# Optimization experiments

Hardware: AMD Instinct MI355X
Metric: run time of the kernel (lower is better)

## Reference

```python
import jax, jax.numpy as jnp
import numpy as np

N = 50000      # nodes
E = 600000     # edges
CIN = 256      # in_channels
H = 4          # heads
C = 64         # hidden_channels (per head)
RATIO = 0.5
K1 = int(np.ceil(RATIO * N))   # 25000
K2 = int(np.ceil(RATIO * K1))  # 12500
NEG = jnp.float32(-1e30)


def gat_conv(x, src, dst, mask, W, a_src, a_dst, b, n):
    """PyG GATConv (concat=True, add_self_loops=True, negative_slope=0.2).
    x: [n, Fin]; src/dst: [e]; mask: [e] bool (invalid edges excluded)."""
    h = (x @ W).reshape(n, H, C)                    # [n, H, C]
    loop = jnp.arange(n, dtype=src.dtype)
    src = jnp.concatenate([src, loop])
    dst = jnp.concatenate([dst, loop])
    mask = jnp.concatenate([mask, jnp.ones((n,), bool)])
    al_s = jnp.sum(h * a_src, axis=-1)              # [n, H]
    al_d = jnp.sum(h * a_dst, axis=-1)              # [n, H]
    e = jax.nn.leaky_relu(al_s[src] + al_d[dst], negative_slope=0.2)  # [e', H]
    e = jnp.where(mask[:, None], e, NEG)
    m = jax.ops.segment_max(e, dst, num_segments=n)                   # [n, H]
    ex = jnp.where(mask[:, None], jnp.exp(e - m[dst]), 0.0)
    den = jax.ops.segment_sum(ex, dst, num_segments=n)                # [n, H]
    alpha = ex / den[dst]                                             # softmax over in-edges
    msg = alpha[:, :, None] * h[src]                                  # [e', H, C]
    out = jax.ops.segment_sum(msg, dst, num_segments=n)               # [n, H, C]
    return out.reshape(n, H * C) + b


def topk_pool(x, src, dst, mask, p, k):
    """PyG TopKPooling: score = tanh(x.p/|p|), keep top-k nodes, gate x by score,
    reindex surviving edges (dropped edges masked out)."""
    score = jnp.tanh((x @ p) / jnp.linalg.norm(p))   # [n]
    sc, perm = jax.lax.top_k(score, k)               # descending, like torch.topk
    x_new = x[perm] * sc[:, None]
    n = x.shape[0]
    inv = jnp.full((n,), -1, jnp.int32).at[perm].set(jnp.arange(k, dtype=jnp.int32))
    ns, nd = inv[src], inv[dst]
    nmask = mask & (ns >= 0) & (nd >= 0)
    ns = jnp.where(nmask, ns, 0)
    nd = jnp.where(nmask, nd, 0)
    return x_new, ns, nd, nmask, perm


def setup_inputs():
    key = jax.random.key(0)
    ks = jax.random.split(key, 14)
    s = 0.05
    return {
        "x": jax.random.normal(ks[0], (N, CIN), jnp.float32),
        "edge_index": jax.random.randint(ks[1], (2, E), 0, N, dtype=jnp.int32),
        "batch": jnp.zeros((N,), jnp.int32),
        "W1": jax.random.normal(ks[2], (CIN, H * C), jnp.float32) * s,
        "a_src1": jax.random.normal(ks[3], (H, C), jnp.float32) * s,
        "a_dst1": jax.random.normal(ks[4], (H, C), jnp.float32) * s,
        "b1": jnp.zeros((H * C,), jnp.float32),
        "p1": jax.random.normal(ks[5], (H * C,), jnp.float32) * s,
        "W2": jax.random.normal(ks[6], (H * C, H * C), jnp.float32) * s,
        "a_src2": jax.random.normal(ks[7], (H, C), jnp.float32) * s,
        "a_dst2": jax.random.normal(ks[8], (H, C), jnp.float32) * s,
        "b2": jnp.zeros((H * C,), jnp.float32),
        "p2": jax.random.normal(ks[9], (H * C,), jnp.float32) * s,
    }


def reference(x, edge_index, batch, W1, a_src1, a_dst1, b1, p1,
              W2, a_src2, a_dst2, b2, p2):
    src, dst = edge_index[0], edge_index[1]
    mask = jnp.ones((E,), bool)
    x1 = gat_conv(x, src, dst, mask, W1, a_src1, a_dst1, b1, N)
    x1, src, dst, mask, perm1 = topk_pool(x1, src, dst, mask, p1, K1)
    x1 = jax.nn.relu(x1)
    batch1 = batch[perm1]
    x2 = gat_conv(x1, src, dst, mask, W2, a_src2, a_dst2, b2, K1)
    x2, src, dst, mask, perm2 = topk_pool(x2, src, dst, mask, p2, K2)
    x2 = jax.nn.relu(x2)
    batch2 = batch1[perm2]
    return (x2, jnp.stack([src, dst]), mask, batch2)
```

## Files before the change

kernel.cpp:

```cpp
#include <hip/hip_runtime.h>
#include <math.h>

typedef unsigned long long ull;

#define NN1 50000
#define EE  600000
#define KK1 25000
#define KK2 12500

#define NB (1<<18)
#define BSHIFT 46

#define CDIV(a,b) (((a)+(b)-1)/(b))

__device__ __forceinline__ ull encd(double d){
  ull u = (ull)__double_as_longlong(d);
  return (u & 0x8000000000000000ULL) ? ~u : (u | 0x8000000000000000ULL);
}
__device__ __forceinline__ double lrelu(double z){ return z > 0.0 ? z : 0.2*z; }

__global__ void zeroi_k(int* __restrict__ p, int n){
  int t = blockIdx.x*blockDim.x + threadIdx.x;
  if (t < n) p[t] = 0;
}
__global__ void zero2_k(int* __restrict__ a, int* __restrict__ b, int n){
  int t = blockIdx.x*blockDim.x + threadIdx.x;
  if (t < n){ a[t] = 0; b[t] = 0; }
}

__global__ void prepq_k(const float* __restrict__ W, const float* __restrict__ as,
                        const float* __restrict__ ad, const float* __restrict__ p,
                        double* __restrict__ Q){
  int k = blockIdx.x; int ch = threadIdx.x; int head = ch>>6; int lane = ch&63;
  double w = (double)W[k*256 + ch];
  double vs = w*(double)as[ch], vd = w*(double)ad[ch], vp = w*(double)p[ch];
  for (int off=32; off; off>>=1){
    vs += __shfl_down(vs,off); vd += __shfl_down(vd,off); vp += __shfl_down(vp,off);
  }
  if (lane==0){ Q[k*12+head]=vs; Q[k*12+4+head]=vd; Q[k*12+8+head]=vp; }
}

template<typename TA>
__global__ __launch_bounds__(256) void matvec_k(const TA* __restrict__ A, const double* __restrict__ Q,
                                                double* __restrict__ als, double* __restrict__ ald,
                                                double* __restrict__ hp, int n){
  __shared__ double P[4][64][13];
  int tid = threadIdx.x;
  int w = tid >> 6, l = tid & 63;
  int base = blockIdx.x*64;
  int r = base + l;
  double acc[12];
  #pragma unroll
  for (int j=0;j<12;j++) acc[j] = 0.0;
  if (r < n){
    const TA*    rowp = A + (size_t)r*256 + w*64;
    const double* qp  = Q + (size_t)w*64*12;
    if constexpr (sizeof(TA)==4){
      #pragma unroll 4
      for (int i=0;i<16;i++){
        float4 v = *reinterpret_cast<const float4*>(rowp + i*4);
        double e0=(double)v.x, e1=(double)v.y, e2=(double)v.z, e3=(double)v.w;
        #pragma unroll
        for (int j=0;j<12;j++) acc[j] = fma(e0, qp[(i*4+0)*12+j], acc[j]);
        #pragma unroll
        for (int j=0;j<12;j++) acc[j] = fma(e1, qp[(i*4+1)*12+j], acc[j]);
        #pragma unroll
        for (int j=0;j<12;j++) acc[j] = fma(e2, qp[(i*4+2)*12+j], acc[j]);
        #pragma unroll
        for (int j=0;j<12;j++) acc[j] = fma(e3, qp[(i*4+3)*12+j], acc[j]);
      }
    } else {
      #pragma unroll 4
      for (int i=0;i<32;i++){
        double2 v = *reinterpret_cast<const double2*>(rowp + i*2);
        #pragma unroll
        for (int j=0;j<12;j++) acc[j] = fma(v.x, qp[(i*2+0)*12+j], acc[j]);
        #pragma unroll
        for (int j=0;j<12;j++) acc[j] = fma(v.y, qp[(i*2+1)*12+j], acc[j]);
      }
    }
  }
  #pragma unroll
  for (int j=0;j<12;j++) P[w][l][j] = acc[j];
  __syncthreads();
  if (tid < 64){
    int rr = base + tid;
    if (rr < n){
      double s[12];
      #pragma unroll
      for (int j=0;j<12;j++)
        s[j] = ((P[0][tid][j] + P[1][tid][j]) + P[2][tid][j]) + P[3][tid][j];
      #pragma unroll
      for (int h=0;h<4;h++){
        als[rr*4+h] = s[h];
        ald[rr*4+h] = s[4+h];
        hp [rr*4+h] = s[8+h];
      }
    }
  }
}

__global__ void deg_k(const int* __restrict__ dst, const int* __restrict__ msk,
                      int* __restrict__ deg, int e){
  int t = blockIdx.x*blockDim.x + threadIdx.x;
  if (t >= e) return;
  if (msk && !msk[t]) return;
  atomicAdd(&deg[dst[t]], 1);
}

__global__ __launch_bounds__(256) void scanA_k(int* __restrict__ a, int* __restrict__ btot, int n){
  __shared__ int s[256];
  int g = blockIdx.x*256 + threadIdx.x;
  s[threadIdx.x] = (g < n) ? a[g] : 0;
  __syncthreads();
  for (int off=1; off<256; off<<=1){
    int t = (threadIdx.x >= off) ? s[threadIdx.x-off] : 0;
    __syncthreads();
    s[threadIdx.x] += t;
    __syncthreads();
  }
  if (g < n) a[g] = s[threadIdx.x];
  if (threadIdx.x == 255) btot[blockIdx.x] = s[255];
}

__global__ __launch_bounds__(1024) void scanB_k(int* __restrict__ btot, int nb){
  __shared__ int s[1024];
  int t = threadIdx.x;
  s[t] = (t < nb) ? btot[t] : 0;
  __syncthreads();
  for (int off=1; off<1024; off<<=1){
    int v = (t >= off) ? s[t-off] : 0;
    __syncthreads();
    s[t] += v;
    __syncthreads();
  }
  if (t < nb) btot[t] = s[t];
}

__global__ void scanC_rowptr_k(const int* __restrict__ a, const int* __restrict__ btot,
                               int* __restrict__ rowptr, int* __restrict__ cursor, int n){
  int g = blockIdx.x*blockDim.x + threadIdx.x;
  if (g >= n) return;
  int B = g >> 8;
  int off = (B > 0) ? btot[B-1] : 0;
  rowptr[g+1] = a[g] + off;
  cursor[g] = 0;
  if (g == 0) rowptr[0] = 0;
}

__global__ void scanC_above_k(const int* __restrict__ a, const int* __restrict__ btot,
                              int* __restrict__ habove, int nelems, int nbins){
  int g = blockIdx.x*blockDim.x + threadIdx.x;
  if (g >= nbins) return;
  int B = g >> 8;
  int off = (B > 0) ? btot[B-1] : 0;
  habove[g] = nelems - (a[g] + off);
}

__global__ void place_k(const int* __restrict__ dst, const int* __restrict__ msk,
                        const int* __restrict__ src, const int* __restrict__ rowptr,
                        int* __restrict__ cursor, int* __restrict__ csr, int e){
  int t = blockIdx.x*blockDim.x + threadIdx.x;
  if (t >= e) return;
  if (msk && !msk[t]) return;
  int d = dst[t];
  int slot = atomicAdd(&cursor[d], 1);
  csr[rowptr[d] + slot] = src[t];
}

__global__ void nodew_k(const double* __restrict__ als, const double* __restrict__ ald,
                        const double* __restrict__ hp, const int* __restrict__ csr,
                        const int* __restrict__ rowptr, const double* __restrict__ nrmbp,
                        double* __restrict__ wse, double* __restrict__ wed,
                        double* __restrict__ z, int n){
  int g = blockIdx.x*blockDim.x + threadIdx.x;
  int i = g>>2, h = g&3;
  if (i >= n) return;
  double aldv = ald[g];
  double selfev = lrelu(als[g] + aldv);
  int b = rowptr[i], e = rowptr[i+1];
  double m = selfev;
  for (int t=b; t<e; t++){
    int s = csr[t];
    double ev = lrelu(als[s*4+h] + aldv);
    m = fmax(m, ev);
  }
  double ws = exp(selfev - m);
  wse[g] = ws;
  double acc = ws * hp[g];
  double den = ws;
  for (int t=b; t<e; t++){
    int s = csr[t];
    double ev = lrelu(als[s*4+h] + aldv);
    double w = exp(ev - m);
    wed[(long)t*4+h] = w;
    acc = fma(w, hp[(long)s*4+h], acc);
    den += w;
  }
  double part = acc/den;
  part += __shfl_xor(part, 1);
  part += __shfl_xor(part, 2);
  if (h == 0) z[i] = (part + nrmbp[1]) / nrmbp[0];
}

template<typename TA>
__global__ void aggx4_k(const TA* __restrict__ X, const int* __restrict__ prm,
                        const int* __restrict__ rowptr, const int* __restrict__ csr,
                        const double* __restrict__ wed, const double* __restrict__ wse,
                        double* __restrict__ Xagg){
  int r = blockIdx.x, k = threadIdx.x;
  int i = prm[r];
  double w0 = wse[i*4+0], w1 = wse[i*4+1], w2 = wse[i*4+2], w3 = wse[i*4+3];
  double xv = (double)X[(long)i*256 + k];
  double a0=w0*xv, a1=w1*xv, a2=w2*xv, a3=w3*xv;
  double d0=w0, d1=w1, d2=w2, d3=w3;
  int b = rowptr[i], e = rowptr[i+1];
  for (int t=b; t<e; t++){
    int s = csr[t];
    double sv = (double)X[(long)s*256 + k];
    double e0=wed[(long)t*4+0], e1=wed[(long)t*4+1];
    double e2=wed[(long)t*4+2], e3=wed[(long)t*4+3];
    a0=fma(e0,sv,a0); a1=fma(e1,sv,a1); a2=fma(e2,sv,a2); a3=fma(e3,sv,a3);
    d0+=e0; d1+=e1; d2+=e2; d3+=e3;
  }
  long base = (long)r*1024 + k;
  Xagg[base      ] = a0/d0;
  Xagg[base + 256] = a1/d1;
  Xagg[base + 512] = a2/d2;
  Xagg[base + 768] = a3/d3;
}

template<typename TO>
__global__ __launch_bounds__(256) void gemmE_k(const double* __restrict__ A,
                                               const float* __restrict__ W,
                                               const float* __restrict__ bias,
                                               const double* __restrict__ scs,
                                               TO* __restrict__ Out, int n){
  __shared__ double As[64][34];
  __shared__ double Bs[32][68];
  int tid = threadIdx.x;
  int r0 = blockIdx.x*64; int head = blockIdx.y; int c0 = head*64;
  int ty = tid>>4, tx = tid&15;
  double acc[4][4] = {};
  for (int k0=0; k0<256; k0+=32){
    int kA = tid&31, rA = tid>>5;
    #pragma unroll
    for (int i=0;i<8;i++){
      int rr = rA + i*8; int gr = r0+rr;
      As[rr][kA] = (gr<n) ? A[(long)gr*1024 + head*256 + k0 + kA] : 0.0;
    }
    int cB = tid&63, kB = tid>>6;
    #pragma unroll
    for (int i=0;i<8;i++){
      int kk = kB + i*4;
      Bs[kk][cB] = (double)W[(k0+kk)*256 + c0 + cB];
    }
    __syncthreads();
    #pragma unroll 4
    for (int k=0;k<32;k+=2){
      double2 a2[4];
      double blo[4], bhi[4];
      #pragma unroll
      for (int i=0;i<4;i++) a2[i] = *reinterpret_cast<const double2*>(&As[ty*4+i][k]);
      #pragma unroll
      for (int j=0;j<4;j++){ blo[j] = Bs[k][tx+16*j]; bhi[j] = Bs[k+1][tx+16*j]; }
      #pragma unroll
      for (int i=0;i<4;i++)
        #pragma unroll
        for (int j=0;j<4;j++) acc[i][j] = fma(a2[i].x, blo[j], acc[i][j]);
      #pragma unroll
      for (int i=0;i<4;i++)
        #pragma unroll
        for (int j=0;j<4;j++) acc[i][j] = fma(a2[i].y, bhi[j], acc[i][j]);
    }
    __syncthreads();
  }
  #pragma unroll
  for (int i=0;i<4;i++){
    int gr = r0 + ty*4 + i;
    if (gr < n){
      double s = scs[gr];
      #pragma unroll
      for (int j=0;j<4;j++){
        int c = c0 + tx + 16*j;
        double v = (acc[i][j] + (double)bias[c]) * s;
        Out[(long)gr*256 + c] = (TO)(v > 0.0 ? v : 0.0);
      }
    }
  }
}

__global__ void pnorm_k(const float* __restrict__ p, const float* __restrict__ bias,
                        double* __restrict__ nrmbp){
  __shared__ double ws_[8];
  int tid = threadIdx.x;
  double pv = (double)p[tid];
  double v = pv*pv;
  double w = (double)bias[tid]*pv;
  for (int off=32; off; off>>=1){ v += __shfl_down(v, off); w += __shfl_down(w, off); }
  if ((tid&63)==0){ ws_[tid>>6] = v; ws_[4+(tid>>6)] = w; }
  __syncthreads();
  if (tid == 0){
    nrmbp[0] = sqrt(ws_[0]+ws_[1]+ws_[2]+ws_[3]);
    nrmbp[1] = ws_[4]+ws_[5]+ws_[6]+ws_[7];
  }
}

__global__ void keyhist_k(const double* __restrict__ z, ull* __restrict__ k64,
                          int* __restrict__ hist, int n){
  int i = blockIdx.x*blockDim.x + threadIdx.x;
  if (i >= n) return;
  ull e = encd(z[i]);
  k64[i] = e;
  atomicAdd(&hist[(int)(e >> BSHIFT)], 1);
}

__global__ void bplace_k(const ull* __restrict__ k64, const int* __restrict__ habove,
                         int* __restrict__ cur, int* __restrict__ isort, int n){
  int i = blockIdx.x*blockDim.x + threadIdx.x;
  if (i >= n) return;
  int b = (int)(k64[i] >> BSHIFT);
  int slot = atomicAdd(&cur[b], 1);
  isort[habove[b] + slot] = i;
}

__global__ void brank_k(const ull* __restrict__ k64, const int* __restrict__ habove,
                        const int* __restrict__ isort, int* __restrict__ rank, int n){
  int i = blockIdx.x*blockDim.x + threadIdx.x;
  if (i >= n) return;
  ull ki = k64[i];
  int b = (int)(ki >> BSHIFT);
  int lo = habove[b];
  int hi = (b > 0) ? habove[b-1] : n;
  int cnt = 0;
  for (int t = lo; t < hi; t++){
    int j = isort[t];
    ull kj = k64[j];
    cnt += ((kj > ki) || (kj == ki && j < i)) ? 1 : 0;
  }
  rank[i] = lo + cnt;
}

__global__ void scatter_k(const double* __restrict__ z, const int* __restrict__ rank,
                          int* __restrict__ perm, int* __restrict__ inv,
                          double* __restrict__ scs, int n, int k){
  int i = blockIdx.x*blockDim.x + threadIdx.x;
  if (i >= n) return;
  int r = rank[i];
  inv[i] = (r < k) ? r : -1;
  if (r < k){ perm[r] = i; scs[r] = tanh(z[i]); }
}

__global__ void reindex_k(const int* __restrict__ src, const int* __restrict__ dst,
                          const int* __restrict__ inv,
                          int* __restrict__ ns, int* __restrict__ nd, int* __restrict__ nmsk, int e){
  int t = blockIdx.x*blockDim.x + threadIdx.x;
  if (t >= e) return;
  int a = inv[src[t]], b = inv[dst[t]];
  int ok = (a >= 0) && (b >= 0);
  ns[t] = ok ? a : 0; nd[t] = ok ? b : 0; nmsk[t] = ok;
}

__global__ void finedge_k(const int* __restrict__ ns, const int* __restrict__ nd,
                          const int* __restrict__ msk, const int* __restrict__ inv,
                          float* __restrict__ osrc, float* __restrict__ odst,
                          float* __restrict__ omsk, int e){
  int t = blockIdx.x*blockDim.x + threadIdx.x;
  if (t >= e) return;
  int a = inv[ns[t]], b = inv[nd[t]];
  int ok = msk[t] && (a >= 0) && (b >= 0);
  osrc[t] = (float)(ok ? a : 0);
  odst[t] = (float)(ok ? b : 0);
  omsk[t] = ok ? 1.0f : 0.0f;
}

__global__ void zerof_k(float* __restrict__ o, int n){
  int t = blockIdx.x*blockDim.x + threadIdx.x;
  if (t < n) o[t] = 0.0f;
}

extern "C" void kernel_launch(void* const* d_in, const int* in_sizes, int n_in,
                              void* d_out, int out_size, void* d_ws, size_t ws_size,
                              hipStream_t stream){
  (void)in_sizes; (void)n_in; (void)out_size; (void)ws_size;
  const float* x   = (const float*)d_in[0];
  const int*   ei  = (const int*)d_in[1];
  const float* W1  = (const float*)d_in[3];
  const float* as1 = (const float*)d_in[4];
  const float* ad1 = (const float*)d_in[5];
  const float* b1  = (const float*)d_in[6];
  const float* p1  = (const float*)d_in[7];
  const float* W2  = (const float*)d_in[8];
  const float* as2 = (const float*)d_in[9];
  const float* ad2 = (const float*)d_in[10];
  const float* b2  = (const float*)d_in[11];
  const float* p2  = (const float*)d_in[12];
  const int* src0 = ei;
  const int* dst0 = ei + EE;

  char* cur_ = (char*)d_ws;
  auto take = [&](size_t bytes)->void*{ void* p = (void*)cur_; cur_ += (bytes + 255) & ~(size_t)255; return p; };
  double* Xagg = (double*)take((size_t)12500*1024*8);
  double* Xi   = (double*)take((size_t)KK1*256*8);
  double* als  = (double*)take((size_t)NN1*4*8);
  double* ald  = (double*)take((size_t)NN1*4*8);
  ull*    menc = (ull*)   take((size_t)NN1*4*8);
  double* wse  = (double*)take((size_t)NN1*4*8);
  double* hp   = (double*)take((size_t)NN1*4*8);
  double* wed  = (double*)take((size_t)EE*4*8);
  double* sco  = (double*)take((size_t)NN1*8);
  double* scs  = (double*)take((size_t)KK1*8);
  double* nrm  = (double*)take(256);
  double* Q    = (double*)take((size_t)3072*8);
  ull*    k64  = (ull*)   take((size_t)NN1*8);
  int* isort= (int*)take((size_t)NN1*4);
  int* rnk  = (int*)take((size_t)NN1*4);
  int* prm  = (int*)take((size_t)KK1*4);
  int* inv  = (int*)take((size_t)NN1*4);
  int* deg  = (int*)take((size_t)(NN1+1)*4);
  int* rwp  = (int*)take((size_t)(NN1+1)*4);
  int* cursr= (int*)take((size_t)NN1*4);
  int* csr  = (int*)take((size_t)EE*4);
  int* ns   = (int*)take((size_t)EE*4);
  int* nd   = (int*)take((size_t)EE*4);
  int* mk2  = (int*)take((size_t)EE*4);
  int* btot = (int*)take((size_t)1024*4);

  int* hist   = (int*)als;
  int* habove = (int*)ald;
  int* bcur   = (int*)menc;

  float* out = (float*)d_out;
  float* o_x = out;
  float* o_s = out + (size_t)KK2*256;
  float* o_d = o_s + EE;
  float* o_m = o_d + EE;
  float* o_b = o_m + EE;

  prepq_k<<<256,256,0,stream>>>(W1, as1, ad1, p1, Q);
  pnorm_k<<<1,256,0,stream>>>(p1, b1, nrm);
  matvec_k<float><<<CDIV(NN1,64),256,0,stream>>>(x, Q, als, ald, hp, NN1);
  zeroi_k<<<CDIV(NN1,256),256,0,stream>>>(deg, NN1);
  deg_k<<<CDIV(EE,256),256,0,stream>>>(dst0, nullptr, deg, EE);
  scanA_k<<<CDIV(NN1,256),256,0,stream>>>(deg, btot, NN1);
  scanB_k<<<1,1024,0,stream>>>(btot, CDIV(NN1,256));
  scanC_rowptr_k<<<CDIV(NN1,256),256,0,stream>>>(deg, btot, rwp, cursr, NN1);
  place_k<<<CDIV(EE,256),256,0,stream>>>(dst0, nullptr, src0, rwp, cursr, csr, EE);
  nodew_k<<<CDIV(NN1*4,256),256,0,stream>>>(als, ald, hp, csr, rwp, nrm, wse, wed, sco, NN1);

  zero2_k<<<NB/256,256,0,stream>>>(hist, bcur, NB);
  keyhist_k<<<CDIV(NN1,256),256,0,stream>>>(sco, k64, hist, NN1);
  scanA_k<<<NB/256,256,0,stream>>>(hist, btot, NB);
  scanB_k<<<1,1024,0,stream>>>(btot, NB/256);
  scanC_above_k<<<NB/256,256,0,stream>>>(hist, btot, habove, NN1, NB);
  bplace_k<<<CDIV(NN1,256),256,0,stream>>>(k64, habove, bcur, isort, NN1);
  brank_k<<<CDIV(NN1,256),256,0,stream>>>(k64, habove, isort, rnk, NN1);
  scatter_k<<<CDIV(NN1,256),256,0,stream>>>(sco, rnk, prm, inv, scs, NN1, KK1);

  aggx4_k<float><<<12500,256,0,stream>>>(x, prm, rwp, csr, wed, wse, Xagg);
  gemmE_k<double><<<dim3(CDIV(12500,64),4),256,0,stream>>>(Xagg, W1, b1, scs, Xi, 12500);
  aggx4_k<float><<<12500,256,0,stream>>>(x, prm+12500, rwp, csr, wed, wse, Xagg);
  gemmE_k<double><<<dim3(CDIV(12500,64),4),256,0,stream>>>(Xagg, W1, b1, scs+12500,
                                                           Xi+(size_t)12500*256, 12500);
  reindex_k<<<CDIV(EE,256),256,0,stream>>>(src0, dst0, inv, ns, nd, mk2, EE);

  prepq_k<<<256,256,0,stream>>>(W2, as2, ad2, p2, Q);
  pnorm_k<<<1,256,0,stream>>>(p2, b2, nrm);
  matvec_k<double><<<CDIV(KK1,64),256,0,stream>>>(Xi, Q, als, ald, hp, KK1);
  zeroi_k<<<CDIV(KK1,256),256,0,stream>>>(deg, KK1);
  deg_k<<<CDIV(EE,256),256,0,stream>>>(nd, mk2, deg, EE);
  scanA_k<<<CDIV(KK1,256),256,0,stream>>>(deg, btot, KK1);
  scanB_k<<<1,1024,0,stream>>>(btot, CDIV(KK1,256));
  scanC_rowptr_k<<<CDIV(KK1,256),256,0,stream>>>(deg, btot, rwp, cursr, KK1);
  place_k<<<CDIV(EE,256),256,0,stream>>>(nd, mk2, ns, rwp, cursr, csr, EE);
  nodew_k<<<CDIV(KK1*4,256),256,0,stream>>>(als, ald, hp, csr, rwp, nrm, wse, wed, sco, KK1);

  zero2_k<<<NB/256,256,0,stream>>>(hist, bcur, NB);
  keyhist_k<<<CDIV(KK1,256),256,0,stream>>>(sco, k64, hist, KK1);
  scanA_k<<<NB/256,256,0,stream>>>(hist, btot, NB);
  scanB_k<<<1,1024,0,stream>>>(btot, NB/256);
  scanC_above_k<<<NB/256,256,0,stream>>>(hist, btot, habove, KK1, NB);
  bplace_k<<<CDIV(KK1,256),256,0,stream>>>(k64, habove, bcur, isort, KK1);
  brank_k<<<CDIV(KK1,256),256,0,stream>>>(k64, habove, isort, rnk, KK1);
  scatter_k<<<CDIV(KK1,256),256,0,stream>>>(sco, rnk, prm, inv, scs, KK1, KK2);

  aggx4_k<double><<<12500,256,0,stream>>>(Xi, prm, rwp, csr, wed, wse, Xagg);
  gemmE_k<float><<<dim3(CDIV(12500,64),4),256,0,stream>>>(Xagg, W2, b2, scs, o_x, 12500);
  finedge_k<<<CDIV(EE,256),256,0,stream>>>(ns, nd, mk2, inv, o_s, o_d, o_m, EE);
  zerof_k<<<CDIV(KK2,256),256,0,stream>>>(o_b, KK2);
}
```

Before: 779.2 us.

## Fold small zeroing and helper kernels into neighbors; halve gemmE row tile

Removes several tiny launches by merging them into neighbouring kernels. pnorm goes into prepq as an extra block, deg zeroing into matvec, hist and bcur zeroing into place_k, scatter into brank, and output zeroing into finedge. Separately, the gemmE row tile drops from 64 to 32 rows per block to get more blocks on the GPU. The histogram buffer moves onto Xagg so that zeroing it during place_k does not clobber als, which nodew still needs. Risks are aliasing bugs between reused scratch buffers and lower data reuse per gemm block.

```diff
diff --git a/kernel.cpp b/kernel.cpp
--- a/kernel.cpp
+++ b/kernel.cpp
@@ -19,21 +19,28 @@
 }
 __device__ __forceinline__ double lrelu(double z){ return z > 0.0 ? z : 0.2*z; }
 
-__global__ void zeroi_k(int* __restrict__ p, int n){
-  int t = blockIdx.x*blockDim.x + threadIdx.x;
-  if (t < n) p[t] = 0;
-}
-__global__ void zero2_k(int* __restrict__ a, int* __restrict__ b, int n){
-  int t = blockIdx.x*blockDim.x + threadIdx.x;
-  if (t < n){ a[t] = 0; b[t] = 0; }
-}
-
 __global__ void prepq_k(const float* __restrict__ W, const float* __restrict__ as,
                         const float* __restrict__ ad, const float* __restrict__ p,
-                        double* __restrict__ Q){
-  int k = blockIdx.x; int ch = threadIdx.x; int head = ch>>6; int lane = ch&63;
-  double w = (double)W[k*256 + ch];
-  double vs = w*(double)as[ch], vd = w*(double)ad[ch], vp = w*(double)p[ch];
+                        const float* __restrict__ bias, double* __restrict__ Q,
+                        double* __restrict__ nrmbp){
+  int tid = threadIdx.x;
+  if (blockIdx.x == 256){
+    __shared__ double ws_[8];
+    double pv = (double)p[tid];
+    double v = pv*pv;
+    double w = (double)bias[tid]*pv;
+    for (int off=32; off; off>>=1){ v += __shfl_down(v, off); w += __shfl_down(w, off); }
+    if ((tid&63)==0){ ws_[tid>>6] = v; ws_[4+(tid>>6)] = w; }
+    __syncthreads();
+    if (tid == 0){
+      nrmbp[0] = sqrt(ws_[0]+ws_[1]+ws_[2]+ws_[3]);
+      nrmbp[1] = ws_[4]+ws_[5]+ws_[6]+ws_[7];
+    }
+    return;
+  }
+  int k = blockIdx.x; int head = tid>>6; int lane = tid&63;
+  double w = (double)W[k*256 + tid];
+  double vs = w*(double)as[tid], vd = w*(double)ad[tid], vp = w*(double)p[tid];
   for (int off=32; off; off>>=1){
     vs += __shfl_down(vs,off); vd += __shfl_down(vd,off); vp += __shfl_down(vp,off);
   }
@@ -43,7 +50,7 @@
 template<typename TA>
 __global__ __launch_bounds__(256) void matvec_k(const TA* __restrict__ A, const double* __restrict__ Q,
                                                 double* __restrict__ als, double* __restrict__ ald,
-                                                double* __restrict__ hp, int n){
+                                                double* __restrict__ hp, int* __restrict__ deg, int n){
   __shared__ double P[4][64][13];
   int tid = threadIdx.x;
   int w = tid >> 6, l = tid & 63;
@@ -96,6 +103,7 @@
         ald[rr*4+h] = s[4+h];
         hp [rr*4+h] = s[8+h];
       }
+      deg[rr] = 0;
     }
   }
 }
@@ -159,8 +167,10 @@
 
 __global__ void place_k(const int* __restrict__ dst, const int* __restrict__ msk,
                         const int* __restrict__ src, const int* __restrict__ rowptr,
-                        int* __restrict__ cursor, int* __restrict__ csr, int e){
+                        int* __restrict__ cursor, int* __restrict__ csr,
+                        int* __restrict__ hist, int* __restrict__ bcur, int e){
   int t = blockIdx.x*blockDim.x + threadIdx.x;
+  if (t < NB){ hist[t] = 0; bcur[t] = 0; }
   if (t >= e) return;
   if (msk && !msk[t]) return;
   int d = dst[t];
@@ -236,16 +246,16 @@
                                                const float* __restrict__ bias,
                                                const double* __restrict__ scs,
                                                TO* __restrict__ Out, int n){
-  __shared__ double As[64][34];
+  __shared__ double As[32][34];
   __shared__ double Bs[32][68];
   int tid = threadIdx.x;
-  int r0 = blockIdx.x*64; int head = blockIdx.y; int c0 = head*64;
-  int ty = tid>>4, tx = tid&15;
-  double acc[4][4] = {};
+  int r0 = blockIdx.x*32; int head = blockIdx.y; int c0 = head*64;
+  int tr = tid>>4, tc = tid&15;
+  double acc[2][4] = {};
   for (int k0=0; k0<256; k0+=32){
     int kA = tid&31, rA = tid>>5;
     #pragma unroll
-    for (int i=0;i<8;i++){
+    for (int i=0;i<4;i++){
       int rr = rA + i*8; int gr = r0+rr;
       As[rr][kA] = (gr<n) ? A[(long)gr*1024 + head*256 + k0 + kA] : 0.0;
     }
@@ -258,51 +268,35 @@
     __syncthreads();
     #pragma unroll 4
     for (int k=0;k<32;k+=2){
-      double2 a2[4];
+      double2 a2[2];
       double blo[4], bhi[4];
       #pragma unroll
-      for (int i=0;i<4;i++) a2[i] = *reinterpret_cast<const double2*>(&As[ty*4+i][k]);
-      #pragma unroll
-      for (int j=0;j<4;j++){ blo[j] = Bs[k][tx+16*j]; bhi[j] = Bs[k+1][tx+16*j]; }
-      #pragma unroll
-      for (int i=0;i<4;i++)
+      for (int i=0;i<2;i++) a2[i] = *reinterpret_cast<const double2*>(&As[tr*2+i][k]);
+      #pragma unroll
+      for (int j=0;j<4;j++){ blo[j] = Bs[k][tc+16*j]; bhi[j] = Bs[k+1][tc+16*j]; }
+      #pragma unroll
+      for (int i=0;i<2;i++)
         #pragma unroll
         for (int j=0;j<4;j++) acc[i][j] = fma(a2[i].x, blo[j], acc[i][j]);
       #pragma unroll
-      for (int i=0;i<4;i++)
+      for (int i=0;i<2;i++)
         #pragma unroll
         for (int j=0;j<4;j++) acc[i][j] = fma(a2[i].y, bhi[j], acc[i][j]);
     }
     __syncthreads();
   }
   #pragma unroll
-  for (int i=0;i<4;i++){
-    int gr = r0 + ty*4 + i;
+  for (int i=0;i<2;i++){
+    int gr = r0 + tr*2 + i;
     if (gr < n){
       double s = scs[gr];
       #pragma unroll
       for (int j=0;j<4;j++){
-        int c = c0 + tx + 16*j;
+        int c = c0 + tc + 16*j;
         double v = (acc[i][j] + (double)bias[c]) * s;
         Out[(long)gr*256 + c] = (TO)(v > 0.0 ? v : 0.0);
       }
     }
-  }
-}
-
-__global__ void pnorm_k(const float* __restrict__ p, const float* __restrict__ bias,
-                        double* __restrict__ nrmbp){
-  __shared__ double ws_[8];
-  int tid = threadIdx.x;
-  double pv = (double)p[tid];
-  double v = pv*pv;
-  double w = (double)bias[tid]*pv;
-  for (int off=32; off; off>>=1){ v += __shfl_down(v, off); w += __shfl_down(w, off); }
-  if ((tid&63)==0){ ws_[tid>>6] = v; ws_[4+(tid>>6)] = w; }
-  __syncthreads();
-  if (tid == 0){
-    nrmbp[0] = sqrt(ws_[0]+ws_[1]+ws_[2]+ws_[3]);
-    nrmbp[1] = ws_[4]+ws_[5]+ws_[6]+ws_[7];
   }
 }
 
@@ -325,7 +319,9 @@
 }
 
 __global__ void brank_k(const ull* __restrict__ k64, const int* __restrict__ habove,
-                        const int* __restrict__ isort, int* __restrict__ rank, int n){
+                        const int* __restrict__ isort, const double* __restrict__ z,
+                        int* __restrict__ perm, int* __restrict__ inv,
+                        double* __restrict__ scs, int n, int kk){
   int i = blockIdx.x*blockDim.x + threadIdx.x;
   if (i >= n) return;
   ull ki = k64[i];
@@ -338,17 +334,9 @@
     ull kj = k64[j];
     cnt += ((kj > ki) || (kj == ki && j < i)) ? 1 : 0;
   }
-  rank[i] = lo + cnt;
-}
-
-__global__ void scatter_k(const double* __restrict__ z, const int* __restrict__ rank,
-                          int* __restrict__ perm, int* __restrict__ inv,
-                          double* __restrict__ scs, int n, int k){
-  int i = blockIdx.x*blockDim.x + threadIdx.x;
-  if (i >= n) return;
-  int r = rank[i];
-  inv[i] = (r < k) ? r : -1;
-  if (r < k){ perm[r] = i; scs[r] = tanh(z[i]); }
+  int r = lo + cnt;
+  inv[i] = (r < kk) ? r : -1;
+  if (r < kk){ perm[r] = i; scs[r] = tanh(z[i]); }
 }
 
 __global__ void reindex_k(const int* __restrict__ src, const int* __restrict__ dst,
@@ -364,19 +352,15 @@
 __global__ void finedge_k(const int* __restrict__ ns, const int* __restrict__ nd,
                           const int* __restrict__ msk, const int* __restrict__ inv,
                           float* __restrict__ osrc, float* __restrict__ odst,
-                          float* __restrict__ omsk, int e){
+                          float* __restrict__ omsk, float* __restrict__ ob, int e){
   int t = blockIdx.x*blockDim.x + threadIdx.x;
+  if (t < KK2) ob[t] = 0.0f;
   if (t >= e) return;
   int a = inv[ns[t]], b = inv[nd[t]];
   int ok = msk[t] && (a >= 0) && (b >= 0);
   osrc[t] = (float)(ok ? a : 0);
   odst[t] = (float)(ok ? b : 0);
   omsk[t] = ok ? 1.0f : 0.0f;
-}
-
-__global__ void zerof_k(float* __restrict__ o, int n){
-  int t = blockIdx.x*blockDim.x + threadIdx.x;
-  if (t < n) o[t] = 0.0f;
 }
 
 extern "C" void kernel_launch(void* const* d_in, const int* in_sizes, int n_in,
@@ -414,7 +398,6 @@
   double* Q    = (double*)take((size_t)3072*8);
   ull*    k64  = (ull*)   take((size_t)NN1*8);
   int* isort= (int*)take((size_t)NN1*4);
-  int* rnk  = (int*)take((size_t)NN1*4);
   int* prm  = (int*)take((size_t)KK1*4);
   int* inv  = (int*)take((size_t)NN1*4);
   int* deg  = (int*)take((size_t)(NN1+1)*4);
@@ -426,7 +409,7 @@
   int* mk2  = (int*)take((size_t)EE*4);
   int* btot = (int*)take((size_t)1024*4);
 
-  int* hist   = (int*)als;
+  int* hist   = (int*)Xagg;
   int* habove = (int*)ald;
   int* bcur   = (int*)menc;
 
@@ -437,55 +420,46 @@
   float* o_m = o_d + EE;
   float* o_b = o_m + EE;
 
-  prepq_k<<<256,256,0,stream>>>(W1, as1, ad1, p1, Q);
-  pnorm_k<<<1,256,0,stream>>>(p1, b1, nrm);
-  matvec_k<float><<<CDIV(NN1,64),256,0,stream>>>(x, Q, als, ald, hp, NN1);
-  zeroi_k<<<CDIV(NN1,256),256,0,stream>>>(deg, NN1);
+  prepq_k<<<257,256,0,stream>>>(W1, as1, ad1, p1, b1, Q, nrm);
+  matvec_k<float><<<CDIV(NN1,64),256,0,stream>>>(x, Q, als, ald, hp, deg, NN1);
   deg_k<<<CDIV(EE,256),256,0,stream>>>(dst0, nullptr, deg, EE);
   scanA_k<<<CDIV(NN1,256),256,0,stream>>>(deg, btot, NN1);
   scanB_k<<<1,1024,0,stream>>>(btot, CDIV(NN1,256));
   scanC_rowptr_k<<<CDIV(NN1,256),256,0,stream>>>(deg, btot, rwp, cursr, NN1);
-  place_k<<<CDIV(EE,256),256,0,stream>>>(dst0, nullptr, src0, rwp, cursr, csr, EE);
+  place_k<<<CDIV(EE,256),256,0,stream>>>(dst0, nullptr, src0, rwp, cursr, csr, hist, bcur, EE);
   nodew_k<<<CDIV(NN1*4,256),256,0,stream>>>(als, ald, hp, csr, rwp, nrm, wse, wed, sco, NN1);
 
-  zero2_k<<<NB/256,256,0,stream>>>(hist, bcur, NB);
   keyhist_k<<<CDIV(NN1,256),256,0,stream>>>(sco, k64, hist, NN1);
   scanA_k<<<NB/256,256,0,stream>>>(hist, btot, NB);
   scanB_k<<<1,1024,0,stream>>>(btot, NB/256);
   scanC_above_k<<<NB/256,256,0,stream>>>(hist, btot, habove, NN1, NB);
   bplace_k<<<CDIV(NN1,256),256,0,stream>>>(k64, habove, bcur, isort, NN1);
-  brank_k<<<CDIV(NN1,256),256,0,stream>>>(k64, habove, isort, rnk, NN1);
-  scatter_k<<<CDIV(NN1,256),256,0,stream>>>(sco, rnk, prm, inv, scs, NN1, KK1);
+  brank_k<<<CDIV(NN1,256),256,0,stream>>>(k64, habove, isort, sco, prm, inv, scs, NN1, KK1);
 
   aggx4_k<float><<<12500,256,0,stream>>>(x, prm, rwp, csr, wed, wse, Xagg);
-  gemmE_k<double><<<dim3(CDIV(12500,64),4),256,0,stream>>>(Xagg, W1, b1, scs, Xi, 12500);
+  gemmE_k<double><<<dim3(CDIV(12500,32),4),256,0,stream>>>(Xagg, W1, b1, scs, Xi, 12500);
   aggx4_k<float><<<12500,256,0,stream>>>(x, prm+12500, rwp, csr, wed, wse, Xagg);
-  gemmE_k<double><<<dim3(CDIV(12500,64),4),256,0,stream>>>(Xagg, W1, b1, scs+12500,
+  gemmE_k<double><<<dim3(CDIV(12500,32),4),256,0,stream>>>(Xagg, W1, b1, scs+12500,
                                                            Xi+(size_t)12500*256, 12500);
   reindex_k<<<CDIV(EE,256),256,0,stream>>>(src0, dst0, inv, ns, nd, mk2, EE);
 
-  prepq_k<<<256,256,0,stream>>>(W2, as2, ad2, p2, Q);
-  pnorm_k<<<1,256,0,stream>>>(p2, b2, nrm);
-  matvec_k<double><<<CDIV(KK1,64),256,0,stream>>>(Xi, Q, als, ald, hp, KK1);
-  zeroi_k<<<CDIV(KK1,256),256,0,stream>>>(deg, KK1);
+  prepq_k<<<257,256,0,stream>>>(W2, as2, ad2, p2, b2, Q, nrm);
+  matvec_k<double><<<CDIV(KK1,64),256,0,stream>>>(Xi, Q, als, ald, hp, deg, KK1);
   deg_k<<<CDIV(EE,256),256,0,stream>>>(nd, mk2, deg, EE);
   scanA_k<<<CDIV(KK1,256),256,0,stream>>>(deg, btot, KK1);
   scanB_k<<<1,1024,0,stream>>>(btot, CDIV(KK1,256));
   scanC_rowptr_k<<<CDIV(KK1,256),256,0,stream>>>(deg, btot, rwp, cursr, KK1);
-  place_k<<<CDIV(EE,256),256,0,stream>>>(nd, mk2, ns, rwp, cursr, csr, EE);
+  place_k<<<CDIV(EE,256),256,0,stream>>>(nd, mk2, ns, rwp, cursr, csr, hist, bcur, EE);
   nodew_k<<<CDIV(KK1*4,256),256,0,stream>>>(als, ald, hp, csr, rwp, nrm, wse, wed, sco, KK1);
 
-  zero2_k<<<NB/256,256,0,stream>>>(hist, bcur, NB);
   keyhist_k<<<CDIV(KK1,256),256,0,stream>>>(sco, k64, hist, KK1);
   scanA_k<<<NB/256,256,0,stream>>>(hist, btot, NB);
   scanB_k<<<1,1024,0,stream>>>(btot, NB/256);
   scanC_above_k<<<NB/256,256,0,stream>>>(hist, btot, habove, KK1, NB);
   bplace_k<<<CDIV(KK1,256),256,0,stream>>>(k64, habove, bcur, isort, KK1);
-  brank_k<<<CDIV(KK1,256),256,0,stream>>>(k64, habove, isort, rnk, KK1);
-  scatter_k<<<CDIV(KK1,256),256,0,stream>>>(sco, rnk, prm, inv, scs, KK1, KK2);
+  brank_k<<<CDIV(KK1,256),256,0,stream>>>(k64, habove, isort, sco, prm, inv, scs, KK1, KK2);
 
   aggx4_k<double><<<12500,256,0,stream>>>(Xi, prm, rwp, csr, wed, wse, Xagg);
-  gemmE_k<float><<<dim3(CDIV(12500,64),4),256,0,stream>>>(Xagg, W2, b2, scs, o_x, 12500);
-  finedge_k<<<CDIV(EE,256),256,0,stream>>>(ns, nd, mk2, inv, o_s, o_d, o_m, EE);
-  zerof_k<<<CDIV(KK2,256),256,0,stream>>>(o_b, KK2);
-}
+  gemmE_k<float><<<dim3(CDIV(12500,32),4),256,0,stream>>>(Xagg, W2, b2, scs, o_x, 12500);
+  finedge_k<<<CDIV(EE,256),256,0,stream>>>(ns, nd, mk2, inv, o_s, o_d, o_m, o_b, EE);
+}
```

Measured after the change: 810.7 us. 4.0% more time.
